# Performance work log

Measured on AMD Instinct MI355X. Metric: run time of the kernel, lower is better.

Reference implementation:

```python
import jax, jax.numpy as jnp
import numpy as np

N_NODES = 100000
D_IN = 64
D_OUT = 64
N_EDGES = 1000000
NEG_SLOPE = 0.2  # PyG GATConv default negative_slope


def _glorot(key, shape):
    fan_in, fan_out = shape[0], shape[-1]
    lim = jnp.sqrt(6.0 / (fan_in + fan_out)).astype(jnp.float32)
    return jax.random.uniform(key, shape, jnp.float32, -lim, lim)


def gat_layer(x, edges, W, a_src, a_dst):
    """Single-head GATConv (bias=False, add_self_loops=True), eval mode."""
    n = x.shape[0]
    h = x @ W  # [N, D]
    loops = jnp.arange(n, dtype=edges.dtype)
    src = jnp.concatenate([edges[0], loops])  # self-loops appended
    dst = jnp.concatenate([edges[1], loops])
    # per-edge attention logits
    e = jnp.take(h @ a_src, src) + jnp.take(h @ a_dst, dst)  # [E+N]
    e = jax.nn.leaky_relu(e, NEG_SLOPE)
    # softmax over incoming edges of each destination node
    m = jax.ops.segment_max(e, dst, num_segments=n)
    w = jnp.exp(e - m[dst])
    denom = jax.ops.segment_sum(w, dst, num_segments=n)
    alpha = w / denom[dst]
    # weighted scatter-aggregate of source features
    return jax.ops.segment_sum(alpha[:, None] * h[src], dst, num_segments=n)


def setup_inputs() -> dict:
    key = jax.random.key(0)
    k = jax.random.split(key, 8)
    x = jax.random.normal(k[0], (N_NODES, D_IN), jnp.float32)
    edges = jax.random.randint(k[1], (2, N_EDGES), 0, N_NODES, dtype=jnp.int64)
    W1 = _glorot(k[2], (D_IN, D_IN))
    as1 = _glorot(k[3], (D_IN,))
    ad1 = _glorot(k[4], (D_IN,))
    W2 = _glorot(k[5], (D_IN, D_OUT))
    as2 = _glorot(k[6], (D_OUT,))
    ad2 = _glorot(k[7], (D_OUT,))
    return {"x": x, "edges": edges, "W1": W1, "as1": as1, "ad1": ad1,
            "W2": W2, "as2": as2, "ad2": ad2}


def reference(x, edges, W1, as1, ad1, W2, as2, ad2):
    h = gat_layer(x, edges, W1, as1, ad1)
    # F.dropout(p=0.2) is identity in eval mode
    return gat_layer(h, edges, W2, as2, ad2)
```

## Files before the change

kernel.cpp:

```cpp
#include <hip/hip_runtime.h>

#define NEG_SLOPE 0.2f

typedef unsigned int uint32;

__device__ __forceinline__ uint32 pack2bf(float a, float b) {
    uint32 ua = __float_as_uint(a);
    uint32 ub = __float_as_uint(b);
    ua += 0x7fffu + ((ua >> 16) & 1u);
    ub += 0x7fffu + ((ub >> 16) & 1u);
    return (ua >> 16) | (ub & 0xffff0000u);
}

__global__ void init_deg_kernel(int* __restrict__ deg, int n) {
    int i = blockIdx.x * blockDim.x + threadIdx.x;
    if (i < n) deg[i] = 0;
}


__device__ __forceinline__ void gemm_body(
        const float* __restrict__ X, const float* __restrict__ W,
        const float* __restrict__ a_src, const float* __restrict__ a_dst,
        uint32* __restrict__ Hb, float* __restrict__ S, float* __restrict__ D,
        int n, int tile, float (*Xs)[68], float* Wl) {
    int tid = threadIdx.x;
    int row0 = tile * 64;
    {
        const float4* W4 = reinterpret_cast<const float4*>(W);
        float4* Wl4 = reinterpret_cast<float4*>(Wl);
        for (int i = tid; i < 1024; i += 256) Wl4[i] = W4[i];
    }
    {
        for (int i = tid; i < 1024; i += 256) {
            int r = i >> 4;
            int c4 = (i & 15) * 4;
            int row = row0 + r;
            float4 xv = {0.f, 0.f, 0.f, 0.f};
            if (row < n) xv = *reinterpret_cast<const float4*>(&X[(size_t)row * 64 + c4]);
            *reinterpret_cast<float4*>(&Xs[r][c4]) = xv;
        }
    }
    __syncthreads();

    int c4 = (tid & 15) * 4;
    int r4 = (tid >> 4) * 4;
    float acc[4][4] = {};
    #pragma unroll 4
    for (int k0 = 0; k0 < 64; k0 += 4) {
        float x4[4][4];
        #pragma unroll
        for (int i = 0; i < 4; ++i)
            *reinterpret_cast<float4*>(x4[i]) =
                *reinterpret_cast<const float4*>(&Xs[r4 + i][k0]);
        #pragma unroll
        for (int j = 0; j < 4; ++j) {
            float4 wv = *reinterpret_cast<const float4*>(&Wl[(k0 + j) * 64 + c4]);
            #pragma unroll
            for (int i = 0; i < 4; ++i) {
                acc[i][0] = fmaf(x4[i][j], wv.x, acc[i][0]);
                acc[i][1] = fmaf(x4[i][j], wv.y, acc[i][1]);
                acc[i][2] = fmaf(x4[i][j], wv.z, acc[i][2]);
                acc[i][3] = fmaf(x4[i][j], wv.w, acc[i][3]);
            }
        }
    }
    #pragma unroll
    for (int i = 0; i < 4; ++i) {
        int row = row0 + r4 + i;
        if (row < n) {
            uint2 p;
            p.x = pack2bf(acc[i][0], acc[i][1]);
            p.y = pack2bf(acc[i][2], acc[i][3]);
            *reinterpret_cast<uint2*>(&Hb[(size_t)row * 32 + (c4 >> 1)]) = p;
        }
    }
    float4 av = *reinterpret_cast<const float4*>(&a_src[c4]);
    float4 bv = *reinterpret_cast<const float4*>(&a_dst[c4]);
    #pragma unroll
    for (int i = 0; i < 4; ++i) {
        float ps = acc[i][0] * av.x + acc[i][1] * av.y + acc[i][2] * av.z + acc[i][3] * av.w;
        float pd = acc[i][0] * bv.x + acc[i][1] * bv.y + acc[i][2] * bv.z + acc[i][3] * bv.w;
        #pragma unroll
        for (int o = 1; o < 16; o <<= 1) {
            ps += __shfl_xor(ps, o);
            pd += __shfl_xor(pd, o);
        }
        int row = row0 + r4 + i;
        if ((tid & 15) == 0 && row < n) { S[row] = ps; D[row] = pd; }
    }
}


__global__ __launch_bounds__(256) void gemm_countfill_kernel(
        const float* __restrict__ X, const float* __restrict__ W,
        const float* __restrict__ a_src, const float* __restrict__ a_dst,
        uint32* __restrict__ Hb, float* __restrict__ S, float* __restrict__ D, int n,
        const int* __restrict__ src, const int* __restrict__ dst,
        int* __restrict__ deg, int* __restrict__ csr, int E, int nblkG) {
    __shared__ float Xs[64][68];
    __shared__ float Wl[64 * 64];

    if (blockIdx.x >= nblkG) {
        int i = (blockIdx.x - nblkG) * 256 + threadIdx.x;
        if (i < E) {
            int d = dst[i];
            int p = atomicAdd(&deg[d], 1);
            if (p < 64) csr[((size_t)d << 6) + p] = src[i];
        }
        return;
    }
    gemm_body(X, W, a_src, a_dst, Hb, S, D, n, blockIdx.x, Xs, Wl);
}


__global__ __launch_bounds__(256) void gemm_sd_kernel(
        const float* __restrict__ X, const float* __restrict__ W,
        const float* __restrict__ a_src, const float* __restrict__ a_dst,
        uint32* __restrict__ Hb, float* __restrict__ S, float* __restrict__ D, int n) {
    __shared__ float Xs[64][68];
    __shared__ float Wl[64 * 64];
    gemm_body(X, W, a_src, a_dst, Hb, S, D, n, blockIdx.x, Xs, Wl);
}


__global__ __launch_bounds__(256) void aggregate_kernel(
        const uint32* __restrict__ Hb, const float* __restrict__ S,
        const float* __restrict__ D, const int* __restrict__ degA,
        const int* __restrict__ csr, float* __restrict__ out, int n) {
    int tid = threadIdx.x;
    int lane = tid & 63;
    int sl = lane & 31;
    int seg = lane >> 5;
    int wv_ = tid >> 6;
    int v = blockIdx.x * 8 + wv_ * 2 + seg;
    bool valid = v < n;
    int dg = -1;
    float dv = 0.f;
    if (valid) { dg = degA[v]; dv = D[v]; }
    int tot = dg + 1;

    if (__all(tot <= 32)) {
        int sreg = 0;
        float e = -INFINITY;
        if (sl < tot) {
            int s0 = (sl < dg) ? csr[((size_t)v << 6) + sl] : v;
            sreg = ((unsigned)s0 < (unsigned)n) ? s0 : 0;
            float t = S[sreg] + dv;
            e = (t > 0.f) ? t : NEG_SLOPE * t;
        }
        float m = e;
        #pragma unroll
        for (int o = 16; o > 0; o >>= 1) m = fmaxf(m, __shfl_xor(m, o));
        float w = (sl < tot) ? __expf(e - m) : 0.f;
        float dsum = w;
        #pragma unroll
        for (int o = 16; o > 0; o >>= 1) dsum += __shfl_xor(dsum, o);
        w *= (1.f / dsum);

        int t8 = sl & 7, g = sl >> 3;
        int segbase = seg << 5;
        int dmax = max(tot, __shfl_xor(tot, 32));
        int nit = (dmax + 3) >> 2;

        float av_[8];
        uint4 uv_[8];
        #pragma unroll
        for (int it = 0; it < 8; ++it) {
            av_[it] = 0.f;
            if (it < nit) {
                int jj = (it << 2) + g;
                int jidx = (jj < tot) ? jj : ((tot > 0) ? tot - 1 : 0);
                float a_ = __shfl(w, segbase + jidx);
                int s_ = __shfl(sreg, segbase + jidx);
                av_[it] = (jj < tot) ? a_ : 0.f;
                uv_[it] = *reinterpret_cast<const uint4*>(&Hb[((size_t)s_ << 5) + (t8 << 2)]);
            }
        }
        float acc[8] = {};
        #pragma unroll
        for (int it = 0; it < 8; ++it) {
            if (it < nit) {
                float a = av_[it];
                uint4 u = uv_[it];
                acc[0] = fmaf(a, __uint_as_float(u.x << 16), acc[0]);
                acc[1] = fmaf(a, __uint_as_float(u.x & 0xffff0000u), acc[1]);
                acc[2] = fmaf(a, __uint_as_float(u.y << 16), acc[2]);
                acc[3] = fmaf(a, __uint_as_float(u.y & 0xffff0000u), acc[3]);
                acc[4] = fmaf(a, __uint_as_float(u.z << 16), acc[4]);
                acc[5] = fmaf(a, __uint_as_float(u.z & 0xffff0000u), acc[5]);
                acc[6] = fmaf(a, __uint_as_float(u.w << 16), acc[6]);
                acc[7] = fmaf(a, __uint_as_float(u.w & 0xffff0000u), acc[7]);
            }
        }
        #pragma unroll
        for (int o = 8; o <= 16; o <<= 1) {
            #pragma unroll
            for (int k = 0; k < 8; ++k) acc[k] += __shfl_xor(acc[k], o);
        }
        if (valid && g == 0) {
            float4 o0 = { acc[0], acc[1], acc[2], acc[3] };
            float4 o1 = { acc[4], acc[5], acc[6], acc[7] };
            *reinterpret_cast<float4*>(&out[(size_t)v * 64 + (t8 << 3)]) = o0;
            *reinterpret_cast<float4*>(&out[(size_t)v * 64 + (t8 << 3) + 4]) = o1;
        }
    } else {
        for (int it = 0; it < 2; ++it) {
            int vv = blockIdx.x * 8 + wv_ * 2 + it;
            if (vv >= n) continue;
            int dg2 = degA[vv];
            int dgc = min(dg2, 64);
            float dv2 = D[vv];
            float ts = S[vv] + dv2;
            float eself = (ts > 0.f) ? ts : NEG_SLOPE * ts;
            float m = -INFINITY;
            for (int j = lane; j < dgc; j += 64) {
                int s0 = csr[((size_t)vv << 6) + j];
                s0 = ((unsigned)s0 < (unsigned)n) ? s0 : 0;
                float t = S[s0] + dv2;
                t = (t > 0.f) ? t : NEG_SLOPE * t;
                m = fmaxf(m, t);
            }
            #pragma unroll
            for (int o = 32; o > 0; o >>= 1) m = fmaxf(m, __shfl_xor(m, o));
            m = fmaxf(m, eself);
            float dsum = 0.f;
            for (int j = lane; j < dgc; j += 64) {
                int s0 = csr[((size_t)vv << 6) + j];
                s0 = ((unsigned)s0 < (unsigned)n) ? s0 : 0;
                float t = S[s0] + dv2;
                t = (t > 0.f) ? t : NEG_SLOPE * t;
                dsum += __expf(t - m);
            }
            #pragma unroll
            for (int o = 32; o > 0; o >>= 1) dsum += __shfl_xor(dsum, o);
            dsum += __expf(eself - m);
            float inv = 1.f / dsum;
            int t8 = lane & 7, g8 = lane >> 3;
            float acc[8] = {};
            for (int b = 0; b < dgc; b += 8) {
                int jj = b + g8;
                if (jj < dgc) {
                    int s = csr[((size_t)vv << 6) + jj];
                    s = ((unsigned)s < (unsigned)n) ? s : 0;
                    float t = S[s] + dv2;
                    t = (t > 0.f) ? t : NEG_SLOPE * t;
                    float a = __expf(t - m) * inv;
                    uint4 u = *reinterpret_cast<const uint4*>(&Hb[((size_t)s << 5) + (t8 << 2)]);
                    acc[0] = fmaf(a, __uint_as_float(u.x << 16), acc[0]);
                    acc[1] = fmaf(a, __uint_as_float(u.x & 0xffff0000u), acc[1]);
                    acc[2] = fmaf(a, __uint_as_float(u.y << 16), acc[2]);
                    acc[3] = fmaf(a, __uint_as_float(u.y & 0xffff0000u), acc[3]);
                    acc[4] = fmaf(a, __uint_as_float(u.z << 16), acc[4]);
                    acc[5] = fmaf(a, __uint_as_float(u.z & 0xffff0000u), acc[5]);
                    acc[6] = fmaf(a, __uint_as_float(u.w << 16), acc[6]);
                    acc[7] = fmaf(a, __uint_as_float(u.w & 0xffff0000u), acc[7]);
                }
            }
            if (g8 == 0) {
                float a = __expf(eself - m) * inv;
                uint4 u = *reinterpret_cast<const uint4*>(&Hb[((size_t)vv << 5) + (t8 << 2)]);
                acc[0] = fmaf(a, __uint_as_float(u.x << 16), acc[0]);
                acc[1] = fmaf(a, __uint_as_float(u.x & 0xffff0000u), acc[1]);
                acc[2] = fmaf(a, __uint_as_float(u.y << 16), acc[2]);
                acc[3] = fmaf(a, __uint_as_float(u.y & 0xffff0000u), acc[3]);
                acc[4] = fmaf(a, __uint_as_float(u.z << 16), acc[4]);
                acc[5] = fmaf(a, __uint_as_float(u.z & 0xffff0000u), acc[5]);
                acc[6] = fmaf(a, __uint_as_float(u.w << 16), acc[6]);
                acc[7] = fmaf(a, __uint_as_float(u.w & 0xffff0000u), acc[7]);
            }
            #pragma unroll
            for (int o = 8; o <= 32; o <<= 1) {
                #pragma unroll
                for (int k = 0; k < 8; ++k) acc[k] += __shfl_xor(acc[k], o);
            }
            if (g8 == 0) {
                float4 o0 = { acc[0], acc[1], acc[2], acc[3] };
                float4 o1 = { acc[4], acc[5], acc[6], acc[7] };
                *reinterpret_cast<float4*>(&out[(size_t)vv * 64 + (t8 << 3)]) = o0;
                *reinterpret_cast<float4*>(&out[(size_t)vv * 64 + (t8 << 3) + 4]) = o1;
            }
        }
    }
}


extern "C" void kernel_launch(void* const* d_in, const int* in_sizes, int n_in,
                              void* d_out, int out_size, void* d_ws, size_t ws_size,
                              hipStream_t stream) {
    const float* x   = (const float*)d_in[0];
    const int*   e   = (const int*)d_in[1];
    const float* W1  = (const float*)d_in[2];
    const float* as1 = (const float*)d_in[3];
    const float* ad1 = (const float*)d_in[4];
    const float* W2  = (const float*)d_in[5];
    const float* as2 = (const float*)d_in[6];
    const float* ad2 = (const float*)d_in[7];
    float* out = (float*)d_out;

    const int N = in_sizes[0] / 64;
    const int E = in_sizes[1] / 2;
    const int* src = e;
    const int* dst = e + E;

    uint32* Hb = (uint32*)d_ws;
    float* S   = (float*)(Hb + (size_t)N * 32);
    float* D   = S + N;
    int* deg   = (int*)(D + N);
    int* csr   = deg + N;
    float* z1  = out;

    const int B = 256;
    int nblkN = (N + B - 1) / B;
    int nblkE = (E + B - 1) / B;
    int nblkG = (N + 63) / 64;
    int nblkA = (N + 7) / 8;

    init_deg_kernel<<<nblkN, B, 0, stream>>>(deg, N);

    gemm_countfill_kernel<<<nblkG + nblkE, B, 0, stream>>>(
        x, W1, as1, ad1, Hb, S, D, N, src, dst, deg, csr, E, nblkG);

    aggregate_kernel<<<nblkA, B, 0, stream>>>(Hb, S, D, deg, csr, z1, N);
    gemm_sd_kernel<<<nblkG, B, 0, stream>>>(z1, W2, as2, ad2, Hb, S, D, N);
    aggregate_kernel<<<nblkA, B, 0, stream>>>(Hb, S, D, deg, csr, out, N);
}
```

Measured before the change: 195.7 us.

## Split CSR fill into separate kernel partitioned by destination range

Splits the fused gemm+countfill launch into a standalone count/fill kernel followed by the first GEMM. The count/fill kernel launches 8x the blocks, and each block group handles only edges whose destination falls in one eighth of the node range. The aim is to improve locality of the atomics and CSR writes by having each wave touch only one slice of deg/csr, possibly keeping it cache- or XCD-local. In exchange, dst is read eight times and the GEMM no longer overlaps with the fill.

Result: faster. 164.6 us (-15.9%).

```diff
diff --git a/kernel.cpp b/kernel.cpp
--- a/kernel.cpp
+++ b/kernel.cpp
@@ -18,13 +18,28 @@
 }
 
 
-__device__ __forceinline__ void gemm_body(
+__global__ void countfill_kernel(const int* __restrict__ src,
+                                 const int* __restrict__ dst,
+                                 int* __restrict__ deg, int* __restrict__ csr,
+                                 int E, int N8) {
+    int q = blockIdx.x & 7;
+    int i = (blockIdx.x >> 3) * 256 + threadIdx.x;
+    if (i >= E) return;
+    int d = dst[i];
+    if (d / N8 != q) return;
+    int p = atomicAdd(&deg[d], 1);
+    if (p < 64) csr[((size_t)d << 6) + p] = src[i];
+}
+
+
+__global__ __launch_bounds__(256) void gemm_sd_kernel(
         const float* __restrict__ X, const float* __restrict__ W,
         const float* __restrict__ a_src, const float* __restrict__ a_dst,
-        uint32* __restrict__ Hb, float* __restrict__ S, float* __restrict__ D,
-        int n, int tile, float (*Xs)[68], float* Wl) {
+        uint32* __restrict__ Hb, float* __restrict__ S, float* __restrict__ D, int n) {
+    __shared__ float Xs[64][68];
+    __shared__ float Wl[64 * 64];
     int tid = threadIdx.x;
-    int row0 = tile * 64;
+    int row0 = blockIdx.x * 64;
     {
         const float4* W4 = reinterpret_cast<const float4*>(W);
         float4* Wl4 = reinterpret_cast<float4*>(Wl);
@@ -88,38 +103,6 @@
         int row = row0 + r4 + i;
         if ((tid & 15) == 0 && row < n) { S[row] = ps; D[row] = pd; }
     }
-}
-
-
-__global__ __launch_bounds__(256) void gemm_countfill_kernel(
-        const float* __restrict__ X, const float* __restrict__ W,
-        const float* __restrict__ a_src, const float* __restrict__ a_dst,
-        uint32* __restrict__ Hb, float* __restrict__ S, float* __restrict__ D, int n,
-        const int* __restrict__ src, const int* __restrict__ dst,
-        int* __restrict__ deg, int* __restrict__ csr, int E, int nblkG) {
-    __shared__ float Xs[64][68];
-    __shared__ float Wl[64 * 64];
-
-    if (blockIdx.x >= nblkG) {
-        int i = (blockIdx.x - nblkG) * 256 + threadIdx.x;
-        if (i < E) {
-            int d = dst[i];
-            int p = atomicAdd(&deg[d], 1);
-            if (p < 64) csr[((size_t)d << 6) + p] = src[i];
-        }
-        return;
-    }
-    gemm_body(X, W, a_src, a_dst, Hb, S, D, n, blockIdx.x, Xs, Wl);
-}
-
-
-__global__ __launch_bounds__(256) void gemm_sd_kernel(
-        const float* __restrict__ X, const float* __restrict__ W,
-        const float* __restrict__ a_src, const float* __restrict__ a_dst,
-        uint32* __restrict__ Hb, float* __restrict__ S, float* __restrict__ D, int n) {
-    __shared__ float Xs[64][68];
-    __shared__ float Wl[64 * 64];
-    gemm_body(X, W, a_src, a_dst, Hb, S, D, n, blockIdx.x, Xs, Wl);
 }
 
 
@@ -314,12 +297,12 @@
     int nblkE = (E + B - 1) / B;
     int nblkG = (N + 63) / 64;
     int nblkA = (N + 7) / 8;
+    int N8 = (N + 7) / 8;
 
     init_deg_kernel<<<nblkN, B, 0, stream>>>(deg, N);
-
-    gemm_countfill_kernel<<<nblkG + nblkE, B, 0, stream>>>(
-        x, W1, as1, ad1, Hb, S, D, N, src, dst, deg, csr, E, nblkG);
-
+    countfill_kernel<<<8 * nblkE, B, 0, stream>>>(src, dst, deg, csr, E, N8);
+
+    gemm_sd_kernel<<<nblkG, B, 0, stream>>>(x, W1, as1, ad1, Hb, S, D, N);
     aggregate_kernel<<<nblkA, B, 0, stream>>>(Hb, S, D, deg, csr, z1, N);
     gemm_sd_kernel<<<nblkG, B, 0, stream>>>(z1, W2, as2, ad2, Hb, S, D, N);
     aggregate_kernel<<<nblkA, B, 0, stream>>>(Hb, S, D, deg, csr, out, N);
```
